# Kernel optimization log

Hardware: AMD Instinct MI355X
Metric: run time of the kernel (lower is better)

Reference implementation:

```python
import jax, jax.numpy as jnp
import numpy as np

B, N, E, D = 4, 2048, 4096, 256


def setup_inputs() -> dict:
    key = jax.random.key(0)
    k = jax.random.split(key, 6)
    return {
        "v_in": jax.random.normal(k[0], (B, N, D), dtype=jnp.float32),
        "e_in": jax.random.normal(k[1], (B, E, D), dtype=jnp.float32),
        "u_in": jax.random.normal(k[2], (B, D), dtype=jnp.float32),
        "adj": jax.random.uniform(k[3], (B, N, N), dtype=jnp.float32),
        "conEd": jax.random.uniform(k[4], (B, N, E), dtype=jnp.float32),
        "edgeAdj": jax.random.uniform(k[5], (B, E, E), dtype=jnp.float32),
    }


def reference(v_in, e_in, u_in, adj, conEd, edgeAdj):
    # pool_from_vertices: adj^T @ v  -> [B, N, D]
    pooled_vertices = jnp.einsum("bmn,bmd->bnd", adj, v_in)
    # pool_from_edges: conEd @ e -> [B, N, D]
    pooled_edges = jnp.einsum("bne,bed->bnd", conEd, e_in)
    # pool_from_universal: broadcast u over the node dimension
    v_out = v_in + pooled_vertices + pooled_edges + u_in[:, None, :]
    return (v_out, e_in, u_in, adj, conEd, edgeAdj)
```

## Files before the change

kernel.cpp:

```cpp
#include <hip/hip_runtime.h>
#include <hip/hip_bf16.h>

constexpr int BB = 4;
constexpr int NN = 2048;
constexpr int EE = 4096;
constexpr int DD = 256;

constexpr long VOUT_SZ = (long)BB * NN * DD;
constexpr long E_SZ    = (long)BB * EE * DD;
constexpr long U_SZ    = (long)BB * DD;
constexpr long ADJ_SZ  = (long)BB * NN * NN;
constexpr long CON_SZ  = (long)BB * NN * EE;
constexpr long EADJ_SZ = (long)BB * EE * EE;

constexpr long OUT_E    = VOUT_SZ;
constexpr long OUT_U    = OUT_E + E_SZ;
constexpr long OUT_ADJ  = OUT_U + U_SZ;
constexpr long OUT_CON  = OUT_ADJ + ADJ_SZ;
constexpr long OUT_EADJ = OUT_CON + CON_SZ;

constexpr int  MM_BLOCKS   = 64;
constexpr int  COPY_BLOCKS = 960;
constexpr long NEED_WS     = 33554432L + 4194304L + 8388608L;

using bf16x4 = __attribute__((ext_vector_type(4))) __bf16;
using bf16x8 = __attribute__((ext_vector_type(8))) __bf16;
using f32x4  = __attribute__((ext_vector_type(4))) float;
using f32x4v = __attribute__((ext_vector_type(4))) float;

__global__ __launch_bounds__(256) void prep_kernel(
    const float* __restrict__ v_in, const float* __restrict__ e_in,
    const float* __restrict__ adj,
    __bf16* __restrict__ adjT, __bf16* __restrict__ vT, __bf16* __restrict__ eT,
    float* __restrict__ out)
{
    __shared__ float tile[64][65];

    int bid = blockIdx.x;
    const float* in; __bf16* outT; float* pass; int R, C, t;
    if (bid < 4096)      { in = adj;  outT = adjT; R = NN; C = NN; t = bid;
                           pass = out + OUT_ADJ; }
    else if (bid < 4608) { in = v_in; outT = vT;   R = NN; C = DD; t = bid - 4096;
                           pass = nullptr; }
    else                 { in = e_in; outT = eT;   R = EE; C = DD; t = bid - 4608;
                           pass = out + OUT_E; }

    int perBatch = (R >> 6) * (C >> 6);
    int b  = t / perBatch;
    int tt = t % perBatch;
    int tilesC = C >> 6;
    int tr = tt / tilesC, tc = tt % tilesC;

    const size_t base = (size_t)b * R * C + (size_t)(tr * 64) * C + tc * 64;
    const float* inb  = in + base;
    float*       pb   = pass ? pass + base : nullptr;
    __bf16*     outb  = outT + (size_t)b * R * C + (size_t)(tc * 64) * R + tr * 64;

    int tid = threadIdx.x;
    #pragma unroll
    for (int it = 0; it < 4; ++it) {
        int q = tid + it * 256;
        int r = q >> 4, c4 = (q & 15) << 2;
        f32x4v fv = *reinterpret_cast<const f32x4v*>(&inb[(size_t)r * C + c4]);
        tile[r][c4 + 0] = fv.x; tile[r][c4 + 1] = fv.y;
        tile[r][c4 + 2] = fv.z; tile[r][c4 + 3] = fv.w;
        if (pb) __builtin_nontemporal_store(fv,
                    reinterpret_cast<f32x4v*>(&pb[(size_t)r * C + c4]));
    }
    __syncthreads();
    #pragma unroll
    for (int it = 0; it < 4; ++it) {
        int q = tid + it * 256;
        int c = q >> 4, r4 = (q & 15) << 2;
        bf16x4 h = { (__bf16)tile[r4 + 0][c], (__bf16)tile[r4 + 1][c],
                     (__bf16)tile[r4 + 2][c], (__bf16)tile[r4 + 3][c] };
        *reinterpret_cast<bf16x4*>(&outb[(size_t)c * R + r4]) = h;
    }
}

__global__ __launch_bounds__(512) void mega_kernel(
    const float* __restrict__ v_in, const float* __restrict__ e_in,
    const float* __restrict__ u_in, const float* __restrict__ adj,
    const float* __restrict__ conEd, const float* __restrict__ edgeAdj,
    const __bf16* __restrict__ adjT, const __bf16* __restrict__ vT,
    const __bf16* __restrict__ eT, float* __restrict__ out, long eadjLimit4)
{
    __shared__ __bf16 As[128 * 64];
    __shared__ __bf16 Bs[256 * 64];

    const int bid = blockIdx.x;
    const int tid = threadIdx.x;

    if (bid < MM_BLOCKS) {
        const int b  = bid >> 4;
        const int n0 = (bid & 15) << 7;

        const __bf16* adjT_b = adjT + (size_t)b * NN * NN;
        const __bf16* vT_b   = vT   + (size_t)b * DD * NN;
        const __bf16* eT_b   = eT   + (size_t)b * DD * EE;
        const float*  con_b  = conEd + (size_t)b * NN * EE;
        const float*  v_b    = v_in  + (size_t)b * NN * DD;
        const float*  u_b    = u_in  + (size_t)b * DD;

        const int lane = tid & 63, wid = tid >> 6;
        const int wr = wid >> 2, wc = wid & 3;
        const int lr = lane & 15;
        const int lkq = lane >> 4;

        f32x4 acc[4][4] = {};

        for (int phase = 0; phase < 2; ++phase) {
            const int K = phase ? EE : NN;
            const __bf16* bT = phase ? eT_b : vT_b;
            for (int k0 = 0; k0 < K; k0 += 64) {
                __syncthreads();
                if (phase == 0) {
                    #pragma unroll
                    for (int it = 0; it < 2; ++it) {
                        int q = tid + it * 512;
                        int n = q >> 3, g = q & 7;
                        bf16x8 vv = *reinterpret_cast<const bf16x8*>(
                            &adjT_b[(size_t)(n0 + n) * NN + k0 + (g << 3)]);
                        *reinterpret_cast<bf16x8*>(&As[(n << 6) + ((g ^ (n & 7)) << 3)]) = vv;
                    }
                } else {
                    #pragma unroll
                    for (int it = 0; it < 4; ++it) {
                        int q = tid + it * 512;
                        int n = q >> 4, e4 = (q & 15) << 2;
                        f32x4v fv = *reinterpret_cast<const f32x4v*>(
                            &con_b[(size_t)(n0 + n) * EE + k0 + e4]);
                        bf16x4 h = { (__bf16)fv.x, (__bf16)fv.y, (__bf16)fv.z, (__bf16)fv.w };
                        *reinterpret_cast<bf16x4*>(
                            &As[(n << 6) + (((e4 >> 3) ^ (n & 7)) << 3) + (e4 & 7)]) = h;
                    }
                }
                #pragma unroll
                for (int it = 0; it < 4; ++it) {
                    int q = tid + it * 512;
                    int dd = q >> 3, g = q & 7;
                    bf16x8 vv = *reinterpret_cast<const bf16x8*>(
                        &bT[(size_t)dd * K + k0 + (g << 3)]);
                    *reinterpret_cast<bf16x8*>(&Bs[(dd << 6) + ((g ^ (dd & 7)) << 3)]) = vv;
                }
                __syncthreads();

                #pragma unroll
                for (int ks = 0; ks < 2; ++ks) {
                    const int gk = (ks << 2) + lkq;
                    bf16x8 a[4], bv[4];
                    #pragma unroll
                    for (int i = 0; i < 4; ++i) {
                        int row = (wr << 6) + (i << 4) + lr;
                        a[i] = *reinterpret_cast<const bf16x8*>(
                            &As[(row << 6) + ((gk ^ (row & 7)) << 3)]);
                    }
                    #pragma unroll
                    for (int j = 0; j < 4; ++j) {
                        int col = (wc << 6) + (j << 4) + lr;
                        bv[j] = *reinterpret_cast<const bf16x8*>(
                            &Bs[(col << 6) + ((gk ^ (col & 7)) << 3)]);
                    }
                    #pragma unroll
                    for (int i = 0; i < 4; ++i)
                        #pragma unroll
                        for (int j = 0; j < 4; ++j)
                            acc[i][j] = __builtin_amdgcn_mfma_f32_16x16x32_bf16(
                                a[i], bv[j], acc[i][j], 0, 0, 0);
                }
            }
        }

        float uv[4];
        #pragma unroll
        for (int j = 0; j < 4; ++j) uv[j] = u_b[(wc << 6) + (j << 4) + lr];
        #pragma unroll
        for (int i = 0; i < 4; ++i) {
            #pragma unroll
            for (int r = 0; r < 4; ++r) {
                int n = n0 + (wr << 6) + (i << 4) + (lkq << 2) + r;
                #pragma unroll
                for (int j = 0; j < 4; ++j) {
                    int col = (wc << 6) + (j << 4) + lr;
                    out[((size_t)b * NN + n) * DD + col] =
                        acc[i][j][r] + v_b[(size_t)n * DD + col] + uv[j];
                }
            }
        }
    } else {
        const long i0 = (long)(bid - MM_BLOCKS) * 512 + tid;
        const long stride = (long)COPY_BLOCKS * 512;

        const f32x4v* u4 = reinterpret_cast<const f32x4v*>(u_in);
        f32x4v*      ou4 = reinterpret_cast<f32x4v*>(out + OUT_U);
        for (long i = i0; i < U_SZ / 4; i += stride) ou4[i] = u4[i];

        const f32x4v* c4 = reinterpret_cast<const f32x4v*>(conEd);
        f32x4v*      oc4 = reinterpret_cast<f32x4v*>(out + OUT_CON);
        for (long i = i0; i < CON_SZ / 4; i += stride)
            __builtin_nontemporal_store(__builtin_nontemporal_load(&c4[i]), &oc4[i]);

        const f32x4v* g4 = reinterpret_cast<const f32x4v*>(edgeAdj);
        f32x4v*      og4 = reinterpret_cast<f32x4v*>(out + OUT_EADJ);
        for (long i = i0; i < eadjLimit4; i += stride)
            __builtin_nontemporal_store(__builtin_nontemporal_load(&g4[i]), &og4[i]);
    }
}

__global__ __launch_bounds__(256) void tail_copy_kernel(
    const float* __restrict__ edgeAdj, float* __restrict__ out, long start4)
{
    const long i0 = start4 + (long)blockIdx.x * 256 + threadIdx.x;
    const long stride = (long)gridDim.x * 256;
    const f32x4v* g4 = reinterpret_cast<const f32x4v*>(edgeAdj);
    f32x4v*      og4 = reinterpret_cast<f32x4v*>(out + OUT_EADJ);
    for (long i = i0; i < EADJ_SZ / 4; i += stride)
        __builtin_nontemporal_store(__builtin_nontemporal_load(&g4[i]), &og4[i]);
}

extern "C" void kernel_launch(void* const* d_in, const int* in_sizes, int n_in,
                              void* d_out, int out_size, void* d_ws, size_t ws_size,
                              hipStream_t stream) {
    const float* v_in    = (const float*)d_in[0];
    const float* e_in    = (const float*)d_in[1];
    const float* u_in    = (const float*)d_in[2];
    const float* adj     = (const float*)d_in[3];
    const float* conEd   = (const float*)d_in[4];
    const float* edgeAdj = (const float*)d_in[5];
    float* out = (float*)d_out;

    char* scratch;
    long  eadjLimit4;
    bool  fallback;
    if (ws_size >= (size_t)NEED_WS) {
        scratch = (char*)d_ws;
        eadjLimit4 = EADJ_SZ / 4;
        fallback = false;
    } else {
        long out_bytes = (long)out_size * 4;
        scratch = (char*)d_out + (out_bytes - NEED_WS);
        eadjLimit4 = EADJ_SZ / 4 - NEED_WS / 16;
        fallback = true;
    }
    __bf16* adjT = (__bf16*)(scratch);
    __bf16* vT   = (__bf16*)(scratch + 33554432L);
    __bf16* eT   = (__bf16*)(scratch + 33554432L + 4194304L);

    prep_kernel<<<dim3(5632), dim3(256), 0, stream>>>(
        v_in, e_in, adj, adjT, vT, eT, out);
    mega_kernel<<<dim3(MM_BLOCKS + COPY_BLOCKS), dim3(512), 0, stream>>>(
        v_in, e_in, u_in, adj, conEd, edgeAdj, adjT, vT, eT, out, eadjLimit4);
    if (fallback) {
        tail_copy_kernel<<<dim3(512), dim3(256), 0, stream>>>(
            edgeAdj, out, eadjLimit4);
    }
}
```

Before: 941.5 us.

## Split matmul K dimension across four blocks with atomic accumulation

Splits the combined adj/conEd reduction into four K-chunks per output tile, raising matmul blocks from 64 to 256 so more CUs work on the GEMM. Each partial sum is added to the output with atomics. The v_in+u_in base term is now written by the prep kernel, and the u copy moves there as well. This costs atomic traffic and depends on prep finishing before the atomics run, which stream order guarantees.

Result: faster. 863.3 us (-8.3%).

```diff
diff --git a/kernel.cpp b/kernel.cpp
--- a/kernel.cpp
+++ b/kernel.cpp
@@ -19,8 +19,8 @@
 constexpr long OUT_CON  = OUT_ADJ + ADJ_SZ;
 constexpr long OUT_EADJ = OUT_CON + CON_SZ;
 
-constexpr int  MM_BLOCKS   = 64;
-constexpr int  COPY_BLOCKS = 960;
+constexpr int  MM_BLOCKS   = 256;
+constexpr int  COPY_BLOCKS = 768;
 constexpr long NEED_WS     = 33554432L + 4194304L + 8388608L;
 
 using bf16x4 = __attribute__((ext_vector_type(4))) __bf16;
@@ -30,18 +30,18 @@
 
 __global__ __launch_bounds__(256) void prep_kernel(
     const float* __restrict__ v_in, const float* __restrict__ e_in,
-    const float* __restrict__ adj,
+    const float* __restrict__ u_in, const float* __restrict__ adj,
     __bf16* __restrict__ adjT, __bf16* __restrict__ vT, __bf16* __restrict__ eT,
     float* __restrict__ out)
 {
     __shared__ float tile[64][65];
 
     int bid = blockIdx.x;
-    const float* in; __bf16* outT; float* pass; int R, C, t;
+    const float* in; __bf16* outT; float* pass; int R, C, t; bool isV = false;
     if (bid < 4096)      { in = adj;  outT = adjT; R = NN; C = NN; t = bid;
                            pass = out + OUT_ADJ; }
     else if (bid < 4608) { in = v_in; outT = vT;   R = NN; C = DD; t = bid - 4096;
-                           pass = nullptr; }
+                           pass = nullptr; isV = true; }
     else                 { in = e_in; outT = eT;   R = EE; C = DD; t = bid - 4608;
                            pass = out + OUT_E; }
 
@@ -57,6 +57,12 @@
     __bf16*     outb  = outT + (size_t)b * R * C + (size_t)(tc * 64) * R + tr * 64;
 
     int tid = threadIdx.x;
+
+    if (bid == 4096) {
+        f32x4v uv = reinterpret_cast<const f32x4v*>(u_in)[tid];
+        reinterpret_cast<f32x4v*>(out + OUT_U)[tid] = uv;
+    }
+
     #pragma unroll
     for (int it = 0; it < 4; ++it) {
         int q = tid + it * 256;
@@ -64,8 +70,16 @@
         f32x4v fv = *reinterpret_cast<const f32x4v*>(&inb[(size_t)r * C + c4]);
         tile[r][c4 + 0] = fv.x; tile[r][c4 + 1] = fv.y;
         tile[r][c4 + 2] = fv.z; tile[r][c4 + 3] = fv.w;
-        if (pb) __builtin_nontemporal_store(fv,
-                    reinterpret_cast<f32x4v*>(&pb[(size_t)r * C + c4]));
+        if (pb) {
+            __builtin_nontemporal_store(fv,
+                reinterpret_cast<f32x4v*>(&pb[(size_t)r * C + c4]));
+        } else if (isV) {
+            f32x4v uv = *reinterpret_cast<const f32x4v*>(
+                &u_in[(size_t)b * DD + tc * 64 + c4]);
+            f32x4v s = fv + uv;
+            *reinterpret_cast<f32x4v*>(
+                &out[((size_t)b * NN + tr * 64 + r) * DD + tc * 64 + c4]) = s;
+        }
     }
     __syncthreads();
     #pragma unroll
@@ -92,15 +106,15 @@
     const int tid = threadIdx.x;
 
     if (bid < MM_BLOCKS) {
-        const int b  = bid >> 4;
-        const int n0 = (bid & 15) << 7;
+        const int b  = bid >> 6;
+        const int r  = bid & 63;
+        const int n0 = (r >> 2) << 7;
+        const int kc = r & 3;
 
         const __bf16* adjT_b = adjT + (size_t)b * NN * NN;
         const __bf16* vT_b   = vT   + (size_t)b * DD * NN;
         const __bf16* eT_b   = eT   + (size_t)b * DD * EE;
         const float*  con_b  = conEd + (size_t)b * NN * EE;
-        const float*  v_b    = v_in  + (size_t)b * NN * DD;
-        const float*  u_b    = u_in  + (size_t)b * DD;
 
         const int lane = tid & 63, wid = tid >> 6;
         const int wr = wid >> 2, wc = wid & 3;
@@ -109,91 +123,85 @@
 
         f32x4 acc[4][4] = {};
 
-        for (int phase = 0; phase < 2; ++phase) {
-            const int K = phase ? EE : NN;
+        for (int s = 0; s < 24; ++s) {
+            const int phase = (s >= 8);
+            const int k0 = phase ? kc * 1024 + (s - 8) * 64 : kc * 512 + s * 64;
+            const int K  = phase ? EE : NN;
             const __bf16* bT = phase ? eT_b : vT_b;
-            for (int k0 = 0; k0 < K; k0 += 64) {
-                __syncthreads();
-                if (phase == 0) {
-                    #pragma unroll
-                    for (int it = 0; it < 2; ++it) {
-                        int q = tid + it * 512;
-                        int n = q >> 3, g = q & 7;
-                        bf16x8 vv = *reinterpret_cast<const bf16x8*>(
-                            &adjT_b[(size_t)(n0 + n) * NN + k0 + (g << 3)]);
-                        *reinterpret_cast<bf16x8*>(&As[(n << 6) + ((g ^ (n & 7)) << 3)]) = vv;
-                    }
-                } else {
-                    #pragma unroll
-                    for (int it = 0; it < 4; ++it) {
-                        int q = tid + it * 512;
-                        int n = q >> 4, e4 = (q & 15) << 2;
-                        f32x4v fv = *reinterpret_cast<const f32x4v*>(
-                            &con_b[(size_t)(n0 + n) * EE + k0 + e4]);
-                        bf16x4 h = { (__bf16)fv.x, (__bf16)fv.y, (__bf16)fv.z, (__bf16)fv.w };
-                        *reinterpret_cast<bf16x4*>(
-                            &As[(n << 6) + (((e4 >> 3) ^ (n & 7)) << 3) + (e4 & 7)]) = h;
-                    }
-                }
+
+            __syncthreads();
+            if (!phase) {
+                #pragma unroll
+                for (int it = 0; it < 2; ++it) {
+                    int q = tid + it * 512;
+                    int n = q >> 3, g = q & 7;
+                    bf16x8 vv = *reinterpret_cast<const bf16x8*>(
+                        &adjT_b[(size_t)(n0 + n) * NN + k0 + (g << 3)]);
+                    *reinterpret_cast<bf16x8*>(&As[(n << 6) + ((g ^ (n & 7)) << 3)]) = vv;
+                }
+            } else {
                 #pragma unroll
                 for (int it = 0; it < 4; ++it) {
                     int q = tid + it * 512;
-                    int dd = q >> 3, g = q & 7;
-                    bf16x8 vv = *reinterpret_cast<const bf16x8*>(
-                        &bT[(size_t)dd * K + k0 + (g << 3)]);
-                    *reinterpret_cast<bf16x8*>(&Bs[(dd << 6) + ((g ^ (dd & 7)) << 3)]) = vv;
-                }
-                __syncthreads();
-
-                #pragma unroll
-                for (int ks = 0; ks < 2; ++ks) {
-                    const int gk = (ks << 2) + lkq;
-                    bf16x8 a[4], bv[4];
+                    int n = q >> 4, e4 = (q & 15) << 2;
+                    f32x4v fv = *reinterpret_cast<const f32x4v*>(
+                        &con_b[(size_t)(n0 + n) * EE + k0 + e4]);
+                    bf16x4 h = { (__bf16)fv.x, (__bf16)fv.y, (__bf16)fv.z, (__bf16)fv.w };
+                    *reinterpret_cast<bf16x4*>(
+                        &As[(n << 6) + (((e4 >> 3) ^ (n & 7)) << 3) + (e4 & 7)]) = h;
+                }
+            }
+            #pragma unroll
+            for (int it = 0; it < 4; ++it) {
+                int q = tid + it * 512;
+                int dd = q >> 3, g = q & 7;
+                bf16x8 vv = *reinterpret_cast<const bf16x8*>(
+                    &bT[(size_t)dd * K + k0 + (g << 3)]);
+                *reinterpret_cast<bf16x8*>(&Bs[(dd << 6) + ((g ^ (dd & 7)) << 3)]) = vv;
+            }
+            __syncthreads();
+
+            #pragma unroll
+            for (int ks = 0; ks < 2; ++ks) {
+                const int gk = (ks << 2) + lkq;
+                bf16x8 a[4], bv[4];
+                #pragma unroll
+                for (int i = 0; i < 4; ++i) {
+                    int row = (wr << 6) + (i << 4) + lr;
+                    a[i] = *reinterpret_cast<const bf16x8*>(
+                        &As[(row << 6) + ((gk ^ (row & 7)) << 3)]);
+                }
+                #pragma unroll
+                for (int j = 0; j < 4; ++j) {
+                    int col = (wc << 6) + (j << 4) + lr;
+                    bv[j] = *reinterpret_cast<const bf16x8*>(
+                        &Bs[(col << 6) + ((gk ^ (col & 7)) << 3)]);
+                }
+                #pragma unroll
+                for (int i = 0; i < 4; ++i)
                     #pragma unroll
-                    for (int i = 0; i < 4; ++i) {
-                        int row = (wr << 6) + (i << 4) + lr;
-                        a[i] = *reinterpret_cast<const bf16x8*>(
-                            &As[(row << 6) + ((gk ^ (row & 7)) << 3)]);
-                    }
-                    #pragma unroll
-                    for (int j = 0; j < 4; ++j) {
-                        int col = (wc << 6) + (j << 4) + lr;
-                        bv[j] = *reinterpret_cast<const bf16x8*>(
-                            &Bs[(col << 6) + ((gk ^ (col & 7)) << 3)]);
-                    }
-                    #pragma unroll
-                    for (int i = 0; i < 4; ++i)
-                        #pragma unroll
-                        for (int j = 0; j < 4; ++j)
-                            acc[i][j] = __builtin_amdgcn_mfma_f32_16x16x32_bf16(
-                                a[i], bv[j], acc[i][j], 0, 0, 0);
-                }
+                    for (int j = 0; j < 4; ++j)
+                        acc[i][j] = __builtin_amdgcn_mfma_f32_16x16x32_bf16(
+                            a[i], bv[j], acc[i][j], 0, 0, 0);
             }
         }
 
-        float uv[4];
-        #pragma unroll
-        for (int j = 0; j < 4; ++j) uv[j] = u_b[(wc << 6) + (j << 4) + lr];
         #pragma unroll
         for (int i = 0; i < 4; ++i) {
             #pragma unroll
-            for (int r = 0; r < 4; ++r) {
-                int n = n0 + (wr << 6) + (i << 4) + (lkq << 2) + r;
+            for (int r4 = 0; r4 < 4; ++r4) {
+                int n = n0 + (wr << 6) + (i << 4) + (lkq << 2) + r4;
                 #pragma unroll
                 for (int j = 0; j < 4; ++j) {
                     int col = (wc << 6) + (j << 4) + lr;
-                    out[((size_t)b * NN + n) * DD + col] =
-                        acc[i][j][r] + v_b[(size_t)n * DD + col] + uv[j];
+                    unsafeAtomicAdd(&out[((size_t)b * NN + n) * DD + col],
+                                    acc[i][j][r4]);
                 }
             }
         }
     } else {
         const long i0 = (long)(bid - MM_BLOCKS) * 512 + tid;
         const long stride = (long)COPY_BLOCKS * 512;
-
-        const f32x4v* u4 = reinterpret_cast<const f32x4v*>(u_in);
-        f32x4v*      ou4 = reinterpret_cast<f32x4v*>(out + OUT_U);
-        for (long i = i0; i < U_SZ / 4; i += stride) ou4[i] = u4[i];
 
         const f32x4v* c4 = reinterpret_cast<const f32x4v*>(conEd);
         f32x4v*      oc4 = reinterpret_cast<f32x4v*>(out + OUT_CON);
@@ -239,7 +247,7 @@
     } else {
         long out_bytes = (long)out_size * 4;
         scratch = (char*)d_out + (out_bytes - NEED_WS);
-        eadjLimit4 = EADJ_SZ / 4 - NEED_WS / 16;
+        eadjLimit4 = EADJ_SZ / 4 - (NEED_WS + 15) / 16;
         fallback = true;
     }
     __bf16* adjT = (__bf16*)(scratch);
@@ -247,7 +255,7 @@
     __bf16* eT   = (__bf16*)(scratch + 33554432L + 4194304L);
 
     prep_kernel<<<dim3(5632), dim3(256), 0, stream>>>(
-        v_in, e_in, adj, adjT, vT, eT, out);
+        v_in, e_in, u_in, adj, adjT, vT, eT, out);
     mega_kernel<<<dim3(MM_BLOCKS + COPY_BLOCKS), dim3(512), 0, stream>>>(
         v_in, e_in, u_in, adj, conEd, edgeAdj, adjT, vT, eT, out, eadjLimit4);
     if (fallback) {
```
